# Optimization experiments

Measured on AMD Instinct MI355X. Metric: run time of the kernel, lower is better.

The kernel has to match this reference:

```python
import jax, jax.numpy as jnp
import numpy as np
import math

HIDDEN = 2048
N_HEADS = 16
HEAD = HIDDEN // N_HEADS
B, S = 2, 2048


def setup_inputs() -> dict:
    key = jax.random.key(0)
    k1, k2, k3 = jax.random.split(key, 3)
    scale = 1.0 / math.sqrt(HIDDEN)
    return {
        "x": jax.random.normal(k1, (B, S, HIDDEN), dtype=jnp.float32),
        "w_qkv": jax.random.normal(k2, (HIDDEN, 3 * HIDDEN), dtype=jnp.float32) * scale,
        "b_qkv": jnp.zeros((3 * HIDDEN,), dtype=jnp.float32),
        "w_out": jax.random.normal(k3, (HIDDEN, HIDDEN), dtype=jnp.float32) * scale,
        "b_out": jnp.zeros((HIDDEN,), dtype=jnp.float32),
    }


def reference(x, w_qkv, b_qkv, w_out, b_out):
    b, s, _ = x.shape
    qkv = x @ w_qkv + b_qkv                      # [b, s, 3*hidden]
    q, k, v = jnp.split(qkv, 3, axis=-1)
    # 'b n (h l) -> b h n l'
    def heads(t):
        return t.reshape(b, s, N_HEADS, HEAD).transpose(0, 2, 1, 3)
    q, k, v = heads(q), heads(k), heads(v)
    scores = jnp.einsum("bhql,bhkl->bhqk", q, k) / math.sqrt(HEAD)
    # causal mask: positions where q_ind < k_ind get -10000 (matches source)
    q_ind = jnp.arange(s)[:, None]
    k_ind = jnp.arange(s)[None, :]
    scores = jnp.where(q_ind < k_ind, jnp.float32(-10000.0), scores)
    probs = jax.nn.softmax(scores, axis=-1)
    combined = jnp.einsum("bhqk,bhkl->bhql", probs, v)
    # 'b h q l -> b q (h l)'
    combined = combined.transpose(0, 2, 1, 3).reshape(b, s, HIDDEN)
    return combined @ w_out + b_out
```

## Files before the change

### kernel.cpp

```cpp
#include <hip/hip_runtime.h>
#include <hip/hip_bf16.h>

typedef __attribute__((ext_vector_type(4))) float f32x4;
typedef __attribute__((ext_vector_type(16))) float f32x16;
typedef __attribute__((ext_vector_type(8))) short bf16x8;

#define GBL_AS(p) (const __attribute__((address_space(1))) void*)(p)
#define LDS_AS(p) (__attribute__((address_space(3))) void*)(p)

__device__ __forceinline__ void gload_lds16(const void* g, void* l) {
  __builtin_amdgcn_global_load_lds(GBL_AS(g), LDS_AS(l), 16, 0, 0);
}

__device__ __forceinline__ ushort f2bf(float f) {
  union { float f; unsigned int u; } v; v.f = f;
  unsigned int r = v.u + 0x7fffu + ((v.u >> 16) & 1u);
  return (ushort)(r >> 16);
}

__global__ void cast_f32_bf16_kernel(const float4* __restrict__ in,
                                     ushort4* __restrict__ out, int n4) {
  int i = blockIdx.x * 256 + threadIdx.x;
  if (i < n4) {
    float4 v = in[i];
    ushort4 o;
    o.x = f2bf(v.x); o.y = f2bf(v.y); o.z = f2bf(v.z); o.w = f2bf(v.w);
    out[i] = o;
  }
}

__global__ void transpose_cast_kernel(const float* __restrict__ in,
                                      ushort* __restrict__ out, int R, int C) {
  __shared__ float tile[64][65];
  int tx = threadIdx.x & 63, ty = threadIdx.x >> 6;
  int r0 = blockIdx.y * 64, c0 = blockIdx.x * 64;
#pragma unroll
  for (int i = 0; i < 64; i += 4)
    tile[ty + i][tx] = in[(size_t)(r0 + ty + i) * C + (c0 + tx)];
  __syncthreads();
#pragma unroll
  for (int i = 0; i < 64; i += 4)
    out[(size_t)(c0 + ty + i) * R + (r0 + tx)] = f2bf(tile[tx][ty + i]);
}

template <int MODE>
__global__ __launch_bounds__(256, 2) void gemm_bt_kernel(
    const ushort* __restrict__ A, const ushort* __restrict__ Bt,
    const float* __restrict__ bias, float* __restrict__ C,
    ushort* __restrict__ Qo, ushort* __restrict__ Ko, ushort* __restrict__ Vo,
    int M, int N, int K) {
  __shared__ ushort As[128 * 64];
  __shared__ ushort Bs[128 * 64];
  const int tid = threadIdx.x;
  const int w = tid >> 6, l = tid & 63;
  const int wr = w >> 1, wc = w & 1;
  const int m0 = blockIdx.y * 128, n0 = blockIdx.x * 128;

  f32x4 acc[4][4] = {};

  const int lr = l >> 3;
  const int lc = (l & 7) ^ lr;

  for (int k0 = 0; k0 < K; k0 += 64) {
#pragma unroll
    for (int i = 0; i < 4; ++i) {
      int row = i * 32 + w * 8 + lr;
      gload_lds16(A + (size_t)(m0 + row) * K + k0 + lc * 8,
                  (char*)As + (i * 32 + w * 8) * 128);
      gload_lds16(Bt + (size_t)(n0 + row) * K + k0 + lc * 8,
                  (char*)Bs + (i * 32 + w * 8) * 128);
    }
    __syncthreads();
    const char* Ab = (const char*)As;
    const char* Bb = (const char*)Bs;
#pragma unroll
    for (int ks = 0; ks < 2; ++ks) {
      bf16x8 af[4], bfr[4];
      int cc = ks * 4 + (l >> 4);
#pragma unroll
      for (int mi = 0; mi < 4; ++mi) {
        int row = wr * 64 + mi * 16 + (l & 15);
        af[mi] = *(const bf16x8*)(Ab + row * 128 + ((cc ^ (row & 7)) << 4));
      }
#pragma unroll
      for (int ni = 0; ni < 4; ++ni) {
        int row = wc * 64 + ni * 16 + (l & 15);
        bfr[ni] = *(const bf16x8*)(Bb + row * 128 + ((cc ^ (row & 7)) << 4));
      }
#pragma unroll
      for (int mi = 0; mi < 4; ++mi)
#pragma unroll
        for (int ni = 0; ni < 4; ++ni)
          acc[mi][ni] = __builtin_amdgcn_mfma_f32_16x16x32_bf16(
              af[mi], bfr[ni], acc[mi][ni], 0, 0, 0);
    }
    __syncthreads();
  }

  if (MODE == 0) {
#pragma unroll
    for (int mi = 0; mi < 4; ++mi) {
      int row = m0 + wr * 64 + mi * 16 + ((l >> 4) << 2);
#pragma unroll
      for (int ni = 0; ni < 4; ++ni) {
        int col = n0 + wc * 64 + ni * 16 + (l & 15);
        float b = bias[col];
#pragma unroll
        for (int r = 0; r < 4; ++r)
          C[(size_t)(row + r) * N + col] = acc[mi][ni][r] + b;
      }
    }
  } else {
    const float qscale = 0.08838834764831845f;
#pragma unroll
    for (int ni = 0; ni < 4; ++ni) {
      int n = n0 + wc * 64 + ni * 16 + (l & 15);
      int which = n >> 11;
      int cc2 = n & 2047;
      int h = cc2 >> 7, d = cc2 & 127;
      float b = bias[n];
#pragma unroll
      for (int mi = 0; mi < 4; ++mi) {
        int m = m0 + wr * 64 + mi * 16 + ((l >> 4) << 2);
        int bb = m >> 11, s = m & 2047;
        int bh = bb * 16 + h;
        if (which == 0) {
#pragma unroll
          for (int r = 0; r < 4; ++r)
            Qo[((size_t)bh * 2048 + s + r) * 128 + d] =
                f2bf((acc[mi][ni][r] + b) * qscale);
        } else if (which == 1) {
#pragma unroll
          for (int r = 0; r < 4; ++r)
            Ko[((size_t)bh * 2048 + s + r) * 128 + d] = f2bf(acc[mi][ni][r] + b);
        } else {
          ushort4 pk;
          pk.x = f2bf(acc[mi][ni][0] + b);
          pk.y = f2bf(acc[mi][ni][1] + b);
          pk.z = f2bf(acc[mi][ni][2] + b);
          pk.w = f2bf(acc[mi][ni][3] + b);
          *(ushort4*)(Vo + ((size_t)bh * 128 + d) * 2048 + s) = pk;
        }
      }
    }
  }
}

__global__ __launch_bounds__(512, 2) void attn_kernel(
    const ushort* __restrict__ Qg, const ushort* __restrict__ Kg,
    const ushort* __restrict__ Vtg, ushort* __restrict__ Og) {
  constexpr int S = 2048, D = 128;
  __shared__ ushort Kl[2][64 * 128];
  __shared__ ushort Vl[2][128 * 64];

  const int tid = threadIdx.x, w = tid >> 6, l = tid & 63;
  const int lid = blockIdx.x;
  const int bh = lid & 31;
  const int j = lid >> 5;
  const int g = w >> 2, wv = w & 3;
  const int qb = (g == 0) ? (8 + j) : (7 - j);
  const int wq0 = qb * 128 + wv * 32;
  const int nt_blk = 18 + 2 * j;
  const int ql = l & 31, h32 = l >> 5;

  const ushort* Qb = Qg + (size_t)bh * S * D;
  const ushort* Kb = Kg + (size_t)bh * S * D;
  const ushort* Vb = Vtg + (size_t)bh * D * S;

  bf16x8 qf[8];
#pragma unroll
  for (int ks = 0; ks < 8; ++ks)
    qf[ks] = *(const bf16x8*)(Qb + (size_t)(wq0 + ql) * D + ks * 16 + h32 * 8);

  f32x16 o[4];
#pragma unroll
  for (int dt = 0; dt < 4; ++dt) o[dt] = 0.f;
  float mrun = -1e30f, lrun = 0.f;

  auto stage = [&](int t, int buf) {
    const int k0 = t * 64;
#pragma unroll
    for (int s2 = 0; s2 < 2; ++s2) {
      int i = w * 2 + s2;
      int row = i * 4 + (l >> 4);
      int ck = (l & 15) ^ (row & 7);
      gload_lds16(Kb + (size_t)(k0 + row) * D + ck * 8,
                  (char*)Kl[buf] + i * 1024);
    }
#pragma unroll
    for (int s2 = 0; s2 < 2; ++s2) {
      int i = w * 2 + s2;
      int row = i * 8 + (l >> 3);
      int ck = (l & 7) ^ (row & 7);
      gload_lds16(Vb + (size_t)row * S + k0 + ck * 8,
                  (char*)Vl[buf] + i * 1024);
    }
  };

  stage(0, 0);

  for (int t = 0; t < nt_blk; ++t) {
    const int cur = t & 1;
    const int k0 = t * 64;
    if (t + 1 < nt_blk) {
      stage(t + 1, cur ^ 1);
      asm volatile("s_waitcnt vmcnt(4)" ::: "memory");
    } else {
      asm volatile("s_waitcnt vmcnt(0)" ::: "memory");
    }
    __builtin_amdgcn_s_barrier();

    if (k0 < wq0 + 32) {
      const char* Kc = (const char*)Kl[cur];
      const char* Vc = (const char*)Vl[cur];

      f32x16 sa[2];
#pragma unroll
      for (int kt = 0; kt < 2; ++kt) sa[kt] = 0.f;
      __builtin_amdgcn_s_setprio(1);
#pragma unroll
      for (int kt = 0; kt < 2; ++kt) {
        int row = kt * 32 + ql;
        int swz = row & 7;
#pragma unroll
        for (int ks = 0; ks < 8; ++ks) {
          int c = 2 * ks + h32;
          bf16x8 kf = *(const bf16x8*)(Kc + row * 256 + ((c ^ swz) << 4));
          sa[kt] = __builtin_amdgcn_mfma_f32_32x32x16_bf16(kf, qf[ks], sa[kt],
                                                           0, 0, 0);
        }
      }
      __builtin_amdgcn_s_setprio(0);

      if (k0 + 63 > wq0) {
        int q = wq0 + ql;
#pragma unroll
        for (int kt = 0; kt < 2; ++kt) {
          int kb = k0 + kt * 32 + 4 * h32;
#pragma unroll
          for (int r = 0; r < 16; ++r) {
            int kk = kb + (r & 3) + 8 * (r >> 2);
            if (q < kk) sa[kt][r] = -1e9f;
          }
        }
      }

      float tmax = -1e30f;
#pragma unroll
      for (int kt = 0; kt < 2; ++kt)
#pragma unroll
        for (int r = 0; r < 16; ++r) tmax = fmaxf(tmax, sa[kt][r]);
      tmax = fmaxf(tmax, __shfl_xor(tmax, 32));
      float mnew = fmaxf(mrun, tmax);
      float e = __expf(mrun - mnew);
      float rsum = 0.f;
#pragma unroll
      for (int kt = 0; kt < 2; ++kt)
#pragma unroll
        for (int r = 0; r < 16; ++r) {
          float p = __expf(sa[kt][r] - mnew);
          sa[kt][r] = p;
          rsum += p;
        }
      rsum += __shfl_xor(rsum, 32);
      lrun = lrun * e + rsum;
      mrun = mnew;
#pragma unroll
      for (int dt = 0; dt < 4; ++dt) o[dt] *= e;

#pragma unroll
      for (int kt = 0; kt < 2; ++kt) {
#pragma unroll
        for (int u = 0; u < 2; ++u) {
          int A0, B0, A1, B1;
          asm("v_cvt_pk_bf16_f32 %0, %1, %2"
              : "=v"(A0) : "v"(sa[kt][u * 8 + 0]), "v"(sa[kt][u * 8 + 1]));
          asm("v_cvt_pk_bf16_f32 %0, %1, %2"
              : "=v"(B0) : "v"(sa[kt][u * 8 + 2]), "v"(sa[kt][u * 8 + 3]));
          asm("v_cvt_pk_bf16_f32 %0, %1, %2"
              : "=v"(A1) : "v"(sa[kt][u * 8 + 4]), "v"(sa[kt][u * 8 + 5]));
          asm("v_cvt_pk_bf16_f32 %0, %1, %2"
              : "=v"(B1) : "v"(sa[kt][u * 8 + 6]), "v"(sa[kt][u * 8 + 7]));
          auto r02 = __builtin_amdgcn_permlane32_swap(A0, A1, false, false);
          auto r13 = __builtin_amdgcn_permlane32_swap(B0, B1, false, false);
          union { int i[4]; bf16x8 v; } pu;
          pu.i[0] = r02[0];
          pu.i[1] = r13[0];
          pu.i[2] = r02[1];
          pu.i[3] = r13[1];
          int c = 4 * kt + 2 * u + h32;
          __builtin_amdgcn_s_setprio(1);
#pragma unroll
          for (int dt = 0; dt < 4; ++dt) {
            int row = dt * 32 + ql;
            bf16x8 vf = *(const bf16x8*)(Vc + row * 128 + ((c ^ (row & 7)) << 4));
            o[dt] = __builtin_amdgcn_mfma_f32_32x32x16_bf16(vf, pu.v, o[dt],
                                                            0, 0, 0);
          }
          __builtin_amdgcn_s_setprio(0);
        }
      }
    }
    asm volatile("s_waitcnt lgkmcnt(0)" ::: "memory");
    __builtin_amdgcn_s_barrier();
  }

  const int b = bh >> 4, h = bh & 15;
  float inv = 1.0f / lrun;
  size_t rowbase = ((size_t)b * 2048 + (wq0 + ql)) * 2048 + h * 128;
#pragma unroll
  for (int dt = 0; dt < 4; ++dt)
#pragma unroll
    for (int r4 = 0; r4 < 4; ++r4) {
      int col = dt * 32 + r4 * 8 + h32 * 4;
      ushort4 pk;
      pk.x = f2bf(o[dt][r4 * 4 + 0] * inv);
      pk.y = f2bf(o[dt][r4 * 4 + 1] * inv);
      pk.z = f2bf(o[dt][r4 * 4 + 2] * inv);
      pk.w = f2bf(o[dt][r4 * 4 + 3] * inv);
      *(ushort4*)(Og + rowbase + col) = pk;
    }
}

extern "C" void kernel_launch(void* const* d_in, const int* in_sizes, int n_in,
                              void* d_out, int out_size, void* d_ws,
                              size_t ws_size, hipStream_t stream) {
  const float* x = (const float*)d_in[0];
  const float* w_qkv = (const float*)d_in[1];
  const float* b_qkv = (const float*)d_in[2];
  const float* w_out = (const float*)d_in[3];
  const float* b_out = (const float*)d_in[4];
  float* out = (float*)d_out;
  char* ws = (char*)d_ws;

  if (ws_size < 92274688u) return;
  ushort* xb = (ushort*)(ws);
  ushort* wqkvt = (ushort*)(ws + 16777216);
  ushort* Q = (ushort*)(ws + 41943040);
  ushort* Kb = (ushort*)(ws + 58720256);
  ushort* Vt = (ushort*)(ws + 75497472);
  ushort* comb = xb;
  ushort* woutt = wqkvt;

  cast_f32_bf16_kernel<<<8192, 256, 0, stream>>>((const float4*)x, (ushort4*)xb,
                                                 2097152);
  transpose_cast_kernel<<<dim3(96, 32), 256, 0, stream>>>(w_qkv, wqkvt, 2048,
                                                          6144);
  gemm_bt_kernel<1><<<dim3(48, 32), 256, 0, stream>>>(
      xb, wqkvt, b_qkv, nullptr, Q, Kb, Vt, 4096, 6144, 2048);
  transpose_cast_kernel<<<dim3(32, 32), 256, 0, stream>>>(w_out, woutt, 2048,
                                                          2048);
  attn_kernel<<<dim3(256), 512, 0, stream>>>(Q, Kb, Vt, comb);
  gemm_bt_kernel<0><<<dim3(16, 32), 256, 0, stream>>>(
      comb, woutt, b_out, out, nullptr, nullptr, nullptr, 4096, 2048, 2048);
}
```

Baseline: 233.7 us.

## Replace QKV GEMM with 256x256 double-buffered pipelined kernel and XCD-aware tile swizzle

The QKV projection GEMM moves to a new kernel with 512 threads and 256x256 output tiles. It double-buffers LDS and prefetches the next K-tile's A and B halves while the current MFMA quadrants run, using fine-grained barriers and vmcnt waits. The block index is remapped so neighbouring tiles land on the same XCD, which should improve L2 reuse. Larger tiles cut redundant global loads, at the cost of 128KB of LDS per block, more accumulator registers, lower occupancy and fragile synchronisation.

```diff
diff --git a/kernel.cpp b/kernel.cpp
--- a/kernel.cpp
+++ b/kernel.cpp
@@ -44,95 +44,171 @@
 }
 
 template <int MODE>
-__global__ __launch_bounds__(256, 2) void gemm_bt_kernel(
+__global__ __launch_bounds__(512, 2) void gemm256_kernel(
     const ushort* __restrict__ A, const ushort* __restrict__ Bt,
     const float* __restrict__ bias, float* __restrict__ C,
     ushort* __restrict__ Qo, ushort* __restrict__ Ko, ushort* __restrict__ Vo,
     int M, int N, int K) {
-  __shared__ ushort As[128 * 64];
-  __shared__ ushort Bs[128 * 64];
+  __shared__ ushort lds_buf[2][4][128 * 64];
+
   const int tid = threadIdx.x;
   const int w = tid >> 6, l = tid & 63;
-  const int wr = w >> 1, wc = w & 1;
-  const int m0 = blockIdx.y * 128, n0 = blockIdx.x * 128;
-
-  f32x4 acc[4][4] = {};
-
-  const int lr = l >> 3;
-  const int lc = (l & 7) ^ lr;
-
-  for (int k0 = 0; k0 < K; k0 += 64) {
-#pragma unroll
-    for (int i = 0; i < 4; ++i) {
-      int row = i * 32 + w * 8 + lr;
-      gload_lds16(A + (size_t)(m0 + row) * K + k0 + lc * 8,
-                  (char*)As + (i * 32 + w * 8) * 128);
-      gload_lds16(Bt + (size_t)(n0 + row) * K + k0 + lc * 8,
-                  (char*)Bs + (i * 32 + w * 8) * 128);
-    }
-    __syncthreads();
-    const char* Ab = (const char*)As;
-    const char* Bb = (const char*)Bs;
-#pragma unroll
-    for (int ks = 0; ks < 2; ++ks) {
-      bf16x8 af[4], bfr[4];
-      int cc = ks * 4 + (l >> 4);
-#pragma unroll
-      for (int mi = 0; mi < 4; ++mi) {
-        int row = wr * 64 + mi * 16 + (l & 15);
-        af[mi] = *(const bf16x8*)(Ab + row * 128 + ((cc ^ (row & 7)) << 4));
-      }
+  const int wm = w >> 2, wn = w & 3;
+  const int l15 = l & 15, l4 = l >> 4;
+  const int lr = l >> 3, slot = l & 7;
+  const int lc = slot ^ lr;
+
+  const int nwg = gridDim.x;
+  const int q = nwg >> 3, r = nwg & 7;
+  const int xcd = blockIdx.x & 7, idx = blockIdx.x >> 3;
+  const int swz = (xcd < r ? xcd * (q + 1) : r * (q + 1) + (xcd - r) * q) + idx;
+  const int nby = M >> 8;
+  const int by = swz % nby, bx = swz / nby;
+  const int m0 = by * 256, n0 = bx * 256;
+
+  f32x4 acc[8][4] = {};
+
+  const int NT = K >> 6;
+
+  auto stage_half = [&](const ushort* base, int row0, int kt, int hf) {
+    int buf = kt & 1;
+#pragma unroll
+    for (int s = 0; s < 2; ++s) {
+      int g = w * 2 + s;
+      int row = g * 8 + lr;
+      gload_lds16(base + (size_t)(row0 + row) * K + kt * 64 + lc * 8,
+                  (char*)lds_buf[buf][hf] + g * 1024);
+    }
+  };
+
+  auto rdA4 = [&](bf16x8* a, int buf, int mi0) {
+    const char* Ab = (const char*)lds_buf[buf][wm];
+#pragma unroll
+    for (int mi = 0; mi < 4; ++mi) {
+      int row = (mi0 + mi) * 16 + l15;
+      int sw = row & 7;
+#pragma unroll
+      for (int ks = 0; ks < 2; ++ks) {
+        int c = ks * 4 + l4;
+        a[mi * 2 + ks] = *(const bf16x8*)(Ab + row * 128 + ((c ^ sw) << 4));
+      }
+    }
+  };
+
+  auto rdB2 = [&](bf16x8* b, int buf, int ni0) {
+    const char* Bb = (const char*)lds_buf[buf][2 + (wn >> 1)];
+#pragma unroll
+    for (int ni = 0; ni < 2; ++ni) {
+      int row = (wn & 1) * 64 + (ni0 + ni) * 16 + l15;
+      int sw = row & 7;
+#pragma unroll
+      for (int ks = 0; ks < 2; ++ks) {
+        int c = ks * 4 + l4;
+        b[ni * 2 + ks] = *(const bf16x8*)(Bb + row * 128 + ((c ^ sw) << 4));
+      }
+    }
+  };
+
+  auto quad = [&](const bf16x8* a, const bf16x8* b, int mi0, int ni0) {
+    __builtin_amdgcn_s_setprio(1);
+#pragma unroll
+    for (int mi = 0; mi < 4; ++mi)
+#pragma unroll
+      for (int ni = 0; ni < 2; ++ni)
+#pragma unroll
+        for (int ks = 0; ks < 2; ++ks)
+          acc[mi0 + mi][ni0 + ni] = __builtin_amdgcn_mfma_f32_16x16x32_bf16(
+              a[mi * 2 + ks], b[ni * 2 + ks], acc[mi0 + mi][ni0 + ni], 0, 0, 0);
+    __builtin_amdgcn_s_setprio(0);
+  };
+
+  stage_half(A, m0, 0, 0);
+  stage_half(A, m0 + 128, 0, 1);
+  stage_half(Bt, n0, 0, 2);
+  stage_half(Bt, n0 + 128, 0, 3);
+  if (NT > 1) {
+    stage_half(Bt, n0, 1, 2);
+    stage_half(Bt, n0 + 128, 1, 3);
+  }
+  asm volatile("s_waitcnt vmcnt(4)" ::: "memory");
+  __builtin_amdgcn_s_barrier();
+
+  for (int t = 0; t < NT; ++t) {
+    const int buf = t & 1;
+    bf16x8 a[8], b01[4], b23[4];
+
+    rdA4(a, buf, 0);
+    rdB2(b01, buf, 0);
+    if (t + 1 < NT) stage_half(A, m0, t + 1, 0);
+    __builtin_amdgcn_s_barrier();
+    asm volatile("s_waitcnt lgkmcnt(0)" ::: "memory");
+    __builtin_amdgcn_sched_barrier(0);
+    quad(a, b01, 0, 0);
+    __builtin_amdgcn_s_barrier();
+
+    rdB2(b23, buf, 2);
+    if (t + 1 < NT) stage_half(A, m0 + 128, t + 1, 1);
+    __builtin_amdgcn_s_barrier();
+    asm volatile("s_waitcnt lgkmcnt(0)" ::: "memory");
+    __builtin_amdgcn_sched_barrier(0);
+    quad(a, b23, 0, 2);
+    __builtin_amdgcn_s_barrier();
+
+    rdA4(a, buf, 4);
+    if (t + 2 < NT) stage_half(Bt, n0, t + 2, 2);
+    __builtin_amdgcn_s_barrier();
+    asm volatile("s_waitcnt lgkmcnt(0)" ::: "memory");
+    __builtin_amdgcn_sched_barrier(0);
+    quad(a, b01, 4, 0);
+    __builtin_amdgcn_s_barrier();
+
+    if (t + 2 < NT) {
+      stage_half(Bt, n0 + 128, t + 2, 3);
+      asm volatile("s_waitcnt vmcnt(4)" ::: "memory");
+    } else {
+      asm volatile("s_waitcnt vmcnt(0)" ::: "memory");
+    }
+    __builtin_amdgcn_s_barrier();
+    quad(a, b23, 4, 2);
+    __builtin_amdgcn_s_barrier();
+  }
+
+  if (MODE == 0) {
+#pragma unroll
+    for (int mi = 0; mi < 8; ++mi) {
+      int row = m0 + wm * 128 + mi * 16 + (l4 << 2);
 #pragma unroll
       for (int ni = 0; ni < 4; ++ni) {
-        int row = wc * 64 + ni * 16 + (l & 15);
-        bfr[ni] = *(const bf16x8*)(Bb + row * 128 + ((cc ^ (row & 7)) << 4));
-      }
-#pragma unroll
-      for (int mi = 0; mi < 4; ++mi)
-#pragma unroll
-        for (int ni = 0; ni < 4; ++ni)
-          acc[mi][ni] = __builtin_amdgcn_mfma_f32_16x16x32_bf16(
-              af[mi], bfr[ni], acc[mi][ni], 0, 0, 0);
-    }
-    __syncthreads();
-  }
-
-  if (MODE == 0) {
-#pragma unroll
-    for (int mi = 0; mi < 4; ++mi) {
-      int row = m0 + wr * 64 + mi * 16 + ((l >> 4) << 2);
-#pragma unroll
-      for (int ni = 0; ni < 4; ++ni) {
-        int col = n0 + wc * 64 + ni * 16 + (l & 15);
+        int col = n0 + wn * 64 + ni * 16 + l15;
         float b = bias[col];
 #pragma unroll
-        for (int r = 0; r < 4; ++r)
-          C[(size_t)(row + r) * N + col] = acc[mi][ni][r] + b;
+        for (int rr = 0; rr < 4; ++rr)
+          C[(size_t)(row + rr) * N + col] = acc[mi][ni][rr] + b;
       }
     }
   } else {
     const float qscale = 0.08838834764831845f;
 #pragma unroll
     for (int ni = 0; ni < 4; ++ni) {
-      int n = n0 + wc * 64 + ni * 16 + (l & 15);
+      int n = n0 + wn * 64 + ni * 16 + l15;
       int which = n >> 11;
       int cc2 = n & 2047;
       int h = cc2 >> 7, d = cc2 & 127;
       float b = bias[n];
 #pragma unroll
-      for (int mi = 0; mi < 4; ++mi) {
-        int m = m0 + wr * 64 + mi * 16 + ((l >> 4) << 2);
+      for (int mi = 0; mi < 8; ++mi) {
+        int m = m0 + wm * 128 + mi * 16 + (l4 << 2);
         int bb = m >> 11, s = m & 2047;
         int bh = bb * 16 + h;
         if (which == 0) {
 #pragma unroll
-          for (int r = 0; r < 4; ++r)
-            Qo[((size_t)bh * 2048 + s + r) * 128 + d] =
-                f2bf((acc[mi][ni][r] + b) * qscale);
+          for (int rr = 0; rr < 4; ++rr)
+            Qo[((size_t)bh * 2048 + s + rr) * 128 + d] =
+                f2bf((acc[mi][ni][rr] + b) * qscale);
         } else if (which == 1) {
 #pragma unroll
-          for (int r = 0; r < 4; ++r)
-            Ko[((size_t)bh * 2048 + s + r) * 128 + d] = f2bf(acc[mi][ni][r] + b);
+          for (int rr = 0; rr < 4; ++rr)
+            Ko[((size_t)bh * 2048 + s + rr) * 128 + d] = f2bf(acc[mi][ni][rr] + b);
         } else {
           ushort4 pk;
           pk.x = f2bf(acc[mi][ni][0] + b);
@@ -142,6 +218,73 @@
           *(ushort4*)(Vo + ((size_t)bh * 128 + d) * 2048 + s) = pk;
         }
       }
+    }
+  }
+}
+
+template <int MODE>
+__global__ __launch_bounds__(256, 2) void gemm_bt_kernel(
+    const ushort* __restrict__ A, const ushort* __restrict__ Bt,
+    const float* __restrict__ bias, float* __restrict__ C,
+    int M, int N, int K) {
+  __shared__ ushort As[128 * 64];
+  __shared__ ushort Bs[128 * 64];
+  const int tid = threadIdx.x;
+  const int w = tid >> 6, l = tid & 63;
+  const int wr = w >> 1, wc = w & 1;
+  const int m0 = blockIdx.y * 128, n0 = blockIdx.x * 128;
+
+  f32x4 acc[4][4] = {};
+
+  const int lr = l >> 3;
+  const int lc = (l & 7) ^ lr;
+
+  for (int k0 = 0; k0 < K; k0 += 64) {
+#pragma unroll
+    for (int i = 0; i < 4; ++i) {
+      int row = i * 32 + w * 8 + lr;
+      gload_lds16(A + (size_t)(m0 + row) * K + k0 + lc * 8,
+                  (char*)As + (i * 32 + w * 8) * 128);
+      gload_lds16(Bt + (size_t)(n0 + row) * K + k0 + lc * 8,
+                  (char*)Bs + (i * 32 + w * 8) * 128);
+    }
+    __syncthreads();
+    const char* Ab = (const char*)As;
+    const char* Bb = (const char*)Bs;
+#pragma unroll
+    for (int ks = 0; ks < 2; ++ks) {
+      bf16x8 af[4], bfr[4];
+      int cc = ks * 4 + (l >> 4);
+#pragma unroll
+      for (int mi = 0; mi < 4; ++mi) {
+        int row = wr * 64 + mi * 16 + (l & 15);
+        af[mi] = *(const bf16x8*)(Ab + row * 128 + ((cc ^ (row & 7)) << 4));
+      }
+#pragma unroll
+      for (int ni = 0; ni < 4; ++ni) {
+        int row = wc * 64 + ni * 16 + (l & 15);
+        bfr[ni] = *(const bf16x8*)(Bb + row * 128 + ((cc ^ (row & 7)) << 4));
+      }
+#pragma unroll
+      for (int mi = 0; mi < 4; ++mi)
+#pragma unroll
+        for (int ni = 0; ni < 4; ++ni)
+          acc[mi][ni] = __builtin_amdgcn_mfma_f32_16x16x32_bf16(
+              af[mi], bfr[ni], acc[mi][ni], 0, 0, 0);
+    }
+    __syncthreads();
+  }
+
+#pragma unroll
+  for (int mi = 0; mi < 4; ++mi) {
+    int row = m0 + wr * 64 + mi * 16 + ((l >> 4) << 2);
+#pragma unroll
+    for (int ni = 0; ni < 4; ++ni) {
+      int col = n0 + wc * 64 + ni * 16 + (l & 15);
+      float b = bias[col];
+#pragma unroll
+      for (int rr = 0; rr < 4; ++rr)
+        C[(size_t)(row + rr) * N + col] = acc[mi][ni][rr] + b;
     }
   }
 }
@@ -233,14 +376,14 @@
       __builtin_amdgcn_s_setprio(0);
 
       if (k0 + 63 > wq0) {
-        int q = wq0 + ql;
+        int qq = wq0 + ql;
 #pragma unroll
         for (int kt = 0; kt < 2; ++kt) {
           int kb = k0 + kt * 32 + 4 * h32;
 #pragma unroll
-          for (int r = 0; r < 16; ++r) {
-            int kk = kb + (r & 3) + 8 * (r >> 2);
-            if (q < kk) sa[kt][r] = -1e9f;
+          for (int rr = 0; rr < 16; ++rr) {
+            int kk = kb + (rr & 3) + 8 * (rr >> 2);
+            if (qq < kk) sa[kt][rr] = -1e9f;
           }
         }
       }
@@ -249,7 +392,7 @@
 #pragma unroll
       for (int kt = 0; kt < 2; ++kt)
 #pragma unroll
-        for (int r = 0; r < 16; ++r) tmax = fmaxf(tmax, sa[kt][r]);
+        for (int rr = 0; rr < 16; ++rr) tmax = fmaxf(tmax, sa[kt][rr]);
       tmax = fmaxf(tmax, __shfl_xor(tmax, 32));
       float mnew = fmaxf(mrun, tmax);
       float e = __expf(mrun - mnew);
@@ -257,9 +400,9 @@
 #pragma unroll
       for (int kt = 0; kt < 2; ++kt)
 #pragma unroll
-        for (int r = 0; r < 16; ++r) {
-          float p = __expf(sa[kt][r] - mnew);
-          sa[kt][r] = p;
+        for (int rr = 0; rr < 16; ++rr) {
+          float p = __expf(sa[kt][rr] - mnew);
+          sa[kt][rr] = p;
           rsum += p;
         }
       rsum += __shfl_xor(rsum, 32);
@@ -346,11 +489,11 @@
                                                  2097152);
   transpose_cast_kernel<<<dim3(96, 32), 256, 0, stream>>>(w_qkv, wqkvt, 2048,
                                                           6144);
-  gemm_bt_kernel<1><<<dim3(48, 32), 256, 0, stream>>>(
+  gemm256_kernel<1><<<dim3(384), 512, 0, stream>>>(
       xb, wqkvt, b_qkv, nullptr, Q, Kb, Vt, 4096, 6144, 2048);
   transpose_cast_kernel<<<dim3(32, 32), 256, 0, stream>>>(w_out, woutt, 2048,
                                                           2048);
   attn_kernel<<<dim3(256), 512, 0, stream>>>(Q, Kb, Vt, comb);
   gemm_bt_kernel<0><<<dim3(16, 32), 256, 0, stream>>>(
-      comb, woutt, b_out, out, nullptr, nullptr, nullptr, 4096, 2048, 2048);
-}
+      comb, woutt, b_out, out, 4096, 2048, 2048);
+}
```

Result: slower. 262.0 us (+12.1%).
